# Optimization experiments

Measured on AMD Instinct MI355X. Metric: run time of the kernel, lower is better.

The kernel has to match this reference:

```python
import jax, jax.numpy as jnp
import numpy as np
import math

B, LQ, LK, D = 16, 2048, 2048, 64

def setup_inputs() -> dict:
    key = jax.random.key(0)
    kq, kk, kv, kn = jax.random.split(key, 4)
    q = jax.random.normal(kq, (B, LQ, D), dtype=jnp.float32)
    k = jax.random.normal(kk, (B, LK, D), dtype=jnp.float32)
    v = jax.random.normal(kv, (B, LK, D), dtype=jnp.float32)
    # valid lengths in [1, LK] so no row is fully masked
    valid_num = jax.random.randint(kn, (B,), 1, LK + 1, dtype=jnp.int32)
    return {"q": q, "k": k, "v": v, "valid_num": valid_num}

def reference(q, k, v, valid_num):
    d = q.shape[-1]
    # [B, LQ, LK] scores
    scores = jnp.einsum('bqd,bkd->bqk', q, k) / math.sqrt(d)
    # 1D valid_num -> same key mask for every query row (matches repeat_interleave)
    key_pos = jnp.arange(k.shape[1], dtype=valid_num.dtype)  # [LK]
    mask = key_pos[None, None, :] < valid_num[:, None, None]  # [B,1,LK] -> broadcast
    scores = jnp.where(mask, scores, -jnp.inf)
    attn = jax.nn.softmax(scores, axis=-1)
    # dropout p=0.0 -> identity (eval/deterministic reference)
    return jnp.einsum('bqk,bkd->bqd', attn, v)
```

## Files before the change

kernel.cpp:

```cpp
#include <hip/hip_runtime.h>


namespace {

constexpr int NB  = 16;
constexpr int SLQ = 2048;
constexpr int SLK = 2048;
constexpr int DH  = 64;
constexpr int KB  = 64;
constexpr int QB  = 64;

typedef _Float16 half8  __attribute__((ext_vector_type(8)));
typedef _Float16 half4  __attribute__((ext_vector_type(4)));
typedef _Float16 half2t __attribute__((ext_vector_type(2)));
typedef float    f32x4  __attribute__((ext_vector_type(4)));

__device__ inline half2t pkrtz(float a, float b) {
    return __builtin_bit_cast(half2t, __builtin_amdgcn_cvt_pkrtz(a, b));
}

__global__ __launch_bounds__(256)
void prepass(const float* __restrict__ kg, const float* __restrict__ vg,
             _Float16* __restrict__ k16, _Float16* __restrict__ v16t)
{
    __shared__ _Float16 VT[DH][72];
    const int t  = threadIdx.x;
    const int b  = blockIdx.x >> 5;
    const int kt = blockIdx.x & 31;

    {
        const size_t base = ((size_t)b * SLK + (size_t)kt * KB) * DH;
        const float* kp = kg + base + t * 16;
        f32x4 a0 = ((const f32x4*)kp)[0], a1 = ((const f32x4*)kp)[1];
        f32x4 a2 = ((const f32x4*)kp)[2], a3 = ((const f32x4*)kp)[3];
        union { half2t h2[8]; uint4 u[2]; } o;
        o.h2[0] = pkrtz(a0[0], a0[1]); o.h2[1] = pkrtz(a0[2], a0[3]);
        o.h2[2] = pkrtz(a1[0], a1[1]); o.h2[3] = pkrtz(a1[2], a1[3]);
        o.h2[4] = pkrtz(a2[0], a2[1]); o.h2[5] = pkrtz(a2[2], a2[3]);
        o.h2[6] = pkrtz(a3[0], a3[1]); o.h2[7] = pkrtz(a3[2], a3[3]);
        uint4* dst = (uint4*)(k16 + base + t * 16);
        dst[0] = o.u[0]; dst[1] = o.u[1];
    }
    {
        const int kr = t >> 2, d0 = (t & 3) * 16;
        const float* vp = vg + ((size_t)b * SLK + (size_t)kt * KB + kr) * DH + d0;
        f32x4 a0 = ((const f32x4*)vp)[0], a1 = ((const f32x4*)vp)[1];
        f32x4 a2 = ((const f32x4*)vp)[2], a3 = ((const f32x4*)vp)[3];
#pragma unroll
        for (int i = 0; i < 4; ++i) {
            VT[d0 + i][kr]      = (_Float16)a0[i];
            VT[d0 + 4 + i][kr]  = (_Float16)a1[i];
            VT[d0 + 8 + i][kr]  = (_Float16)a2[i];
            VT[d0 + 12 + i][kr] = (_Float16)a3[i];
        }
    }
    __syncthreads();
#pragma unroll
    for (int j = 0; j < 2; ++j) {
        const int chunk = t * 2 + j;
        const int d = chunk >> 3, c16 = chunk & 7;
        half8 hv = *(const half8*)&VT[d][c16 * 8];
        *(half8*)(v16t + ((size_t)b * DH + d) * SLK + (size_t)kt * KB + c16 * 8) = hv;
    }
}

__global__ __launch_bounds__(256)
void attn_fwd(const float* __restrict__ qg, const _Float16* __restrict__ k16,
              const _Float16* __restrict__ v16t, const int* __restrict__ vn,
              _Float16* __restrict__ ws_acc, float* __restrict__ ws_ml,
              int nsplit, int tps)
{
    __shared__ _Float16 Kl[KB * DH];
    __shared__ _Float16 Vt[DH * KB];

    const int t   = threadIdx.x;
    const int l   = t & 63;
    const int w   = t >> 6;
    const int q15 = l & 15;
    const int g   = l >> 4;
    const int swz = (q15 & 7) << 3;

    const int bid = blockIdx.x;
    int b, qt, s;
    if (nsplit == 8) {
        const int k4 = bid >> 8;
        s  = k4 & 7;
        b  = (((bid >> 4) & 15) + k4) & 15;
        qt = (bid & 15) | ((k4 >> 3) << 4);
    } else {
        b  = ((bid & 15) + 8 * (bid >> 8)) & 15;
        qt = (bid >> 4) & 31;
        s  = 0;
    }

    const int valid = vn[b];
    const int nkt   = (valid + KB - 1) / KB;
    const int kt0   = s * tps;
    if (kt0 >= nkt) return;
    const int kt1   = min(nkt, kt0 + tps);

    const int qrow = qt * QB + w * 16 + q15;

    const float QS = 0.18033688011112042f;

    half8 qf[2];
    {
        const float* qp = qg + ((size_t)b * SLQ + qrow) * DH;
#pragma unroll
        for (int ss = 0; ss < 2; ++ss) {
            const int d0 = 8 * g + 32 * ss;
            f32x4 x = *(const f32x4*)(qp + d0);
            f32x4 y = *(const f32x4*)(qp + d0 + 4);
            half8 h;
#pragma unroll
            for (int i = 0; i < 4; ++i) {
                h[i]     = (_Float16)(x[i] * QS);
                h[i + 4] = (_Float16)(y[i] * QS);
            }
            qf[ss] = h;
        }
    }

    f32x4 acc[4];
#pragma unroll
    for (int i = 0; i < 4; ++i) acc[i] = f32x4{0.f, 0.f, 0.f, 0.f};
    float m = -1e30f, lsum = 0.f;

    const _Float16* k16b = k16 + (size_t)b * SLK * DH;
    const _Float16* v16b = v16t + (size_t)b * DH * SLK;

    const int chunk = 2 * t;
    const int rr_   = chunk >> 3;
    const int cc_   = chunk & 7;
    const int scA   = (cc_ * 8) ^ ((rr_ & 7) << 3);
    const int scB   = scA ^ 8;
    const _Float16* ksrc = k16b + (size_t)chunk * 8;
    const _Float16* vsrc = v16b + (size_t)rr_ * SLK + cc_ * 8;

    uint4 ka, kb, va, vb;
#define PREFETCH(KT)                                                       \
    {                                                                      \
        const _Float16* kp = ksrc + (size_t)(KT) * (KB * DH);              \
        ka = ((const uint4*)kp)[0];                                        \
        kb = ((const uint4*)kp)[1];                                        \
        const _Float16* vp = vsrc + (size_t)(KT) * KB;                     \
        va = ((const uint4*)vp)[0];                                        \
        vb = ((const uint4*)vp)[1];                                        \
    }

    PREFETCH(kt0);

    for (int kt = kt0; kt < kt1; ++kt) {
        __syncthreads();

        *(uint4*)&Kl[rr_ * 64 + scA] = ka;
        *(uint4*)&Kl[rr_ * 64 + scB] = kb;
        *(uint4*)&Vt[rr_ * 64 + scA] = va;
        *(uint4*)&Vt[rr_ * 64 + scB] = vb;
        if (kt + 1 < kt1) PREFETCH(kt + 1);
        __syncthreads();

        f32x4 st[4];
        __builtin_amdgcn_s_setprio(1);
#pragma unroll
        for (int mt = 0; mt < 4; ++mt) {
            f32x4 c = f32x4{0.f, 0.f, 0.f, 0.f};
#pragma unroll
            for (int ss = 0; ss < 2; ++ss) {
                half8 a = *(const half8*)&Kl[(16 * mt + q15) * 64 + ((8 * g + 32 * ss) ^ swz)];
                c = __builtin_amdgcn_mfma_f32_16x16x32_f16(a, qf[ss], c, 0, 0, 0);
            }
            st[mt] = c;
        }
        __builtin_amdgcn_s_setprio(0);

        const int krem = valid - kt * KB;
        if (krem < KB) {
#pragma unroll
            for (int mt = 0; mt < 4; ++mt)
#pragma unroll
                for (int r = 0; r < 4; ++r)
                    if (16 * mt + 4 * g + r >= krem) st[mt][r] = -1e30f;
        }

        float x0 = fmaxf(fmaxf(st[0][0], st[0][1]), fmaxf(st[0][2], st[0][3]));
        float x1 = fmaxf(fmaxf(st[1][0], st[1][1]), fmaxf(st[1][2], st[1][3]));
        float x2 = fmaxf(fmaxf(st[2][0], st[2][1]), fmaxf(st[2][2], st[2][3]));
        float x3 = fmaxf(fmaxf(st[3][0], st[3][1]), fmaxf(st[3][2], st[3][3]));
        float tmax = fmaxf(fmaxf(x0, x1), fmaxf(x2, x3));
        tmax = fmaxf(tmax, __shfl_xor(tmax, 16));
        tmax = fmaxf(tmax, __shfl_xor(tmax, 32));

        if (!__all(tmax - m <= 12.0f)) {
            const float mn = fmaxf(m, tmax);
            const float sc = __builtin_amdgcn_exp2f(m - mn);
            lsum *= sc;
#pragma unroll
            for (int mt = 0; mt < 4; ++mt) acc[mt] *= sc;
            m = mn;
        }

        float p[4][4];
#pragma unroll
        for (int mt = 0; mt < 4; ++mt)
#pragma unroll
            for (int r = 0; r < 4; ++r)
                p[mt][r] = __builtin_amdgcn_exp2f(st[mt][r] - m);

        float s0 = (p[0][0] + p[0][1]) + (p[0][2] + p[0][3]);
        float s1 = (p[1][0] + p[1][1]) + (p[1][2] + p[1][3]);
        float s2 = (p[2][0] + p[2][1]) + (p[2][2] + p[2][3]);
        float s3 = (p[3][0] + p[3][1]) + (p[3][2] + p[3][3]);
        float ps = (s0 + s1) + (s2 + s3);
        ps += __shfl_xor(ps, 16);
        ps += __shfl_xor(ps, 32);
        lsum += ps;

        half2t pk[4][2];
#pragma unroll
        for (int mt = 0; mt < 4; ++mt)
#pragma unroll
            for (int rr = 0; rr < 2; ++rr)
                pk[mt][rr] = pkrtz(p[mt][2 * rr], p[mt][2 * rr + 1]);

        __builtin_amdgcn_s_setprio(1);
#pragma unroll
        for (int ss = 0; ss < 2; ++ss) {
            union { half2t h2[4]; half8 v; } bf;
            bf.h2[0] = pk[2 * ss][0];
            bf.h2[1] = pk[2 * ss][1];
            bf.h2[2] = pk[2 * ss + 1][0];
            bf.h2[3] = pk[2 * ss + 1][1];
#pragma unroll
            for (int mt = 0; mt < 4; ++mt) {
                union { half4 h4[2]; half8 v; } af;
                af.h4[0] = *(const half4*)&Vt[(16 * mt + q15) * 64 + ((32 * ss + 4 * g) ^ swz)];
                af.h4[1] = *(const half4*)&Vt[(16 * mt + q15) * 64 + ((32 * ss + 16 + 4 * g) ^ swz)];
                acc[mt] = __builtin_amdgcn_mfma_f32_16x16x32_f16(af.v, bf.v, acc[mt], 0, 0, 0);
            }
        }
        __builtin_amdgcn_s_setprio(0);
    }
#undef PREFETCH

    const float inv = 1.0f / lsum;
    const size_t row = (size_t)b * SLQ + qrow;
    _Float16* wp = ws_acc + ((size_t)s * NB * SLQ + row) * DH;
#pragma unroll
    for (int mt = 0; mt < 4; ++mt) {
        union { half2t h2[2]; uint2 u; } o;
        o.h2[0] = pkrtz(acc[mt][0] * inv, acc[mt][1] * inv);
        o.h2[1] = pkrtz(acc[mt][2] * inv, acc[mt][3] * inv);
        *(uint2*)(wp + 16 * mt + 4 * g) = o.u;
    }
    if (g == 0)
        *(float2*)(ws_ml + ((size_t)s * NB * SLQ + row) * 2) = make_float2(m, lsum);
}

__global__ __launch_bounds__(256)
void attn_combine(const _Float16* __restrict__ ws_acc, const float* __restrict__ ws_ml,
                  const int* __restrict__ vn, float* __restrict__ og,
                  int nsplit, int tps)
{
    const int tid = blockIdx.x * 256 + threadIdx.x;
    const int row = tid >> 2;
    const int dq  = (tid & 3) << 4;
    const int b   = row >> 11;

    const int valid = vn[b];
    const int nkt   = (valid + KB - 1) / KB;
    const int nact  = min(nsplit, (nkt + tps - 1) / tps);

    float M = -1e30f;
    for (int s = 0; s < nact; ++s)
        M = fmaxf(M, ws_ml[((size_t)s * NB * SLQ + row) * 2]);

    float L = 0.f;
    f32x4 o[4];
#pragma unroll
    for (int i = 0; i < 4; ++i) o[i] = f32x4{0.f, 0.f, 0.f, 0.f};

    for (int s = 0; s < nact; ++s) {
        const float2 ml = *(const float2*)(ws_ml + ((size_t)s * NB * SLQ + row) * 2);
        const float wl = __builtin_amdgcn_exp2f(ml.x - M) * ml.y;
        L += wl;
        const _Float16* ap = ws_acc + ((size_t)s * NB * SLQ + row) * DH + dq;
        half8 h0 = ((const half8*)ap)[0];
        half8 h1 = ((const half8*)ap)[1];
#pragma unroll
        for (int r = 0; r < 4; ++r) {
            o[0][r] += wl * (float)h0[r];
            o[1][r] += wl * (float)h0[4 + r];
            o[2][r] += wl * (float)h1[r];
            o[3][r] += wl * (float)h1[4 + r];
        }
    }

    const float inv = 1.0f / L;
    float* op = og + (size_t)row * DH + dq;
#pragma unroll
    for (int i = 0; i < 4; ++i) {
        f32x4 r = o[i] * inv;
        *(f32x4*)(op + 4 * i) = r;
    }
}

}

extern "C" void kernel_launch(void* const* d_in, const int* in_sizes, int n_in,
                              void* d_out, int out_size, void* d_ws, size_t ws_size,
                              hipStream_t stream)
{
    const float* q    = (const float*)d_in[0];
    const float* k    = (const float*)d_in[1];
    const float* v    = (const float*)d_in[2];
    const int*   vnum = (const int*)d_in[3];
    float* out = (float*)d_out;

    const size_t k16H  = (size_t)NB * SLK * DH;
    const size_t v16H  = k16H;
    const size_t rowsH = (size_t)NB * SLQ;

    int nsplit = 8;
    {
        const size_t need8 = (k16H + v16H + (size_t)8 * rowsH * DH) * 2
                           + (size_t)8 * rowsH * 2 * 4;
        if (ws_size < need8) nsplit = 1;
    }
    const int tps = (nsplit == 8) ? 4 : 32;

    _Float16* k16    = (_Float16*)d_ws;
    _Float16* v16t   = k16 + k16H;
    _Float16* ws_acc = v16t + v16H;
    float*    ws_ml  = (float*)(ws_acc + (size_t)nsplit * rowsH * DH);

    prepass<<<dim3(NB * (SLK / KB)), dim3(256), 0, stream>>>(k, v, k16, v16t);

    dim3 gfwd(nsplit == 8 ? 4096 : 512);
    attn_fwd<<<gfwd, dim3(256), 0, stream>>>(q, k16, v16t, vnum, ws_acc, ws_ml,
                                             nsplit, tps);

    attn_combine<<<dim3((NB * SLQ * 4) / 256), dim3(256), 0, stream>>>(
        ws_acc, ws_ml, vnum, out, nsplit, tps);
}
```

Before: 43.87 us.

## Pre-swizzle K/V tiles in prepass and double-buffer LDS to drop a barrier

The prepass now writes K and transposed V as contiguous 64x64 fp16 tiles with the LDS XOR swizzle already applied. The main kernel can then copy each tile linearly with coalesced uint4 loads and stores. LDS is double-buffered, so each iteration needs one __syncthreads instead of two. This removes per-tile address computation and a barrier, but doubles LDS use to 32 KB per block, which may reduce occupancy.

```diff
diff --git a/kernel.cpp b/kernel.cpp
--- a/kernel.cpp
+++ b/kernel.cpp
@@ -21,25 +21,30 @@
 
 __global__ __launch_bounds__(256)
 void prepass(const float* __restrict__ kg, const float* __restrict__ vg,
-             _Float16* __restrict__ k16, _Float16* __restrict__ v16t)
+             _Float16* __restrict__ kws, _Float16* __restrict__ vws)
 {
     __shared__ _Float16 VT[DH][72];
     const int t  = threadIdx.x;
     const int b  = blockIdx.x >> 5;
     const int kt = blockIdx.x & 31;
+    const size_t tileH = ((size_t)(b << 5) + kt) * 4096;
 
     {
-        const size_t base = ((size_t)b * SLK + (size_t)kt * KB) * DH;
-        const float* kp = kg + base + t * 16;
+        const float* kp = kg + ((size_t)b * SLK + (size_t)kt * KB) * DH + t * 16;
         f32x4 a0 = ((const f32x4*)kp)[0], a1 = ((const f32x4*)kp)[1];
         f32x4 a2 = ((const f32x4*)kp)[2], a3 = ((const f32x4*)kp)[3];
-        union { half2t h2[8]; uint4 u[2]; } o;
-        o.h2[0] = pkrtz(a0[0], a0[1]); o.h2[1] = pkrtz(a0[2], a0[3]);
-        o.h2[2] = pkrtz(a1[0], a1[1]); o.h2[3] = pkrtz(a1[2], a1[3]);
-        o.h2[4] = pkrtz(a2[0], a2[1]); o.h2[5] = pkrtz(a2[2], a2[3]);
-        o.h2[6] = pkrtz(a3[0], a3[1]); o.h2[7] = pkrtz(a3[2], a3[3]);
-        uint4* dst = (uint4*)(k16 + base + t * 16);
-        dst[0] = o.u[0]; dst[1] = o.u[1];
+        union { half2t h2[4]; uint4 u; } o0, o1;
+        o0.h2[0] = pkrtz(a0[0], a0[1]); o0.h2[1] = pkrtz(a0[2], a0[3]);
+        o0.h2[2] = pkrtz(a1[0], a1[1]); o0.h2[3] = pkrtz(a1[2], a1[3]);
+        o1.h2[0] = pkrtz(a2[0], a2[1]); o1.h2[1] = pkrtz(a2[2], a2[3]);
+        o1.h2[2] = pkrtz(a3[0], a3[1]); o1.h2[3] = pkrtz(a3[2], a3[3]);
+#pragma unroll
+        for (int j = 0; j < 2; ++j) {
+            const int n = 2 * t + j;
+            const int rr = n >> 3, c = n & 7;
+            const int dst = rr * 8 + (c ^ (rr & 7));
+            *(uint4*)(kws + tileH + (size_t)dst * 8) = j ? o1.u : o0.u;
+        }
     }
     {
         const int kr = t >> 2, d0 = (t & 3) * 16;
@@ -57,21 +62,21 @@
     __syncthreads();
 #pragma unroll
     for (int j = 0; j < 2; ++j) {
-        const int chunk = t * 2 + j;
-        const int d = chunk >> 3, c16 = chunk & 7;
-        half8 hv = *(const half8*)&VT[d][c16 * 8];
-        *(half8*)(v16t + ((size_t)b * DH + d) * SLK + (size_t)kt * KB + c16 * 8) = hv;
+        const int n = 2 * t + j;
+        const int d = n >> 3, c = n & 7;
+        const int dst = d * 8 + (c ^ (d & 7));
+        half8 hv = *(const half8*)&VT[d][c * 8];
+        *(half8*)(vws + tileH + (size_t)dst * 8) = hv;
     }
 }
 
 __global__ __launch_bounds__(256)
 void attn_fwd(const float* __restrict__ qg, const _Float16* __restrict__ k16,
-              const _Float16* __restrict__ v16t, const int* __restrict__ vn,
+              const _Float16* __restrict__ v16, const int* __restrict__ vn,
               _Float16* __restrict__ ws_acc, float* __restrict__ ws_ml,
               int nsplit, int tps)
 {
-    __shared__ _Float16 Kl[KB * DH];
-    __shared__ _Float16 Vt[DH * KB];
+    __shared__ __attribute__((aligned(16))) _Float16 KV[2][8192];
 
     const int t   = threadIdx.x;
     const int l   = t & 63;
@@ -126,39 +131,35 @@
     for (int i = 0; i < 4; ++i) acc[i] = f32x4{0.f, 0.f, 0.f, 0.f};
     float m = -1e30f, lsum = 0.f;
 
-    const _Float16* k16b = k16 + (size_t)b * SLK * DH;
-    const _Float16* v16b = v16t + (size_t)b * DH * SLK;
-
-    const int chunk = 2 * t;
-    const int rr_   = chunk >> 3;
-    const int cc_   = chunk & 7;
-    const int scA   = (cc_ * 8) ^ ((rr_ & 7) << 3);
-    const int scB   = scA ^ 8;
-    const _Float16* ksrc = k16b + (size_t)chunk * 8;
-    const _Float16* vsrc = v16b + (size_t)rr_ * SLK + cc_ * 8;
-
-    uint4 ka, kb, va, vb;
-#define PREFETCH(KT)                                                       \
-    {                                                                      \
-        const _Float16* kp = ksrc + (size_t)(KT) * (KB * DH);              \
-        ka = ((const uint4*)kp)[0];                                        \
-        kb = ((const uint4*)kp)[1];                                        \
-        const _Float16* vp = vsrc + (size_t)(KT) * KB;                     \
-        va = ((const uint4*)vp)[0];                                        \
-        vb = ((const uint4*)vp)[1];                                        \
-    }
-
-    PREFETCH(kt0);
+    const _Float16* kbase = k16 + (size_t)(b << 5) * 4096;
+    const _Float16* vbase = v16 + (size_t)(b << 5) * 4096;
+
+    uint4 rk0, rk1, rv0, rv1;
+#define LOADREGS(KT)                                                         \
+    {                                                                        \
+        const uint4* kp_ = (const uint4*)(kbase + (size_t)(KT) * 4096);      \
+        const uint4* vp_ = (const uint4*)(vbase + (size_t)(KT) * 4096);      \
+        rk0 = kp_[t]; rk1 = kp_[t + 256];                                    \
+        rv0 = vp_[t]; rv1 = vp_[t + 256];                                    \
+    }
+#define WRITEKV(CUR)                                                         \
+    {                                                                        \
+        uint4* kl_ = (uint4*)&KV[CUR][0];                                    \
+        uint4* vl_ = (uint4*)&KV[CUR][4096];                                 \
+        kl_[t] = rk0; kl_[t + 256] = rk1;                                    \
+        vl_[t] = rv0; vl_[t + 256] = rv1;                                    \
+    }
+
+    LOADREGS(kt0);
+    int cur = 0;
 
     for (int kt = kt0; kt < kt1; ++kt) {
+        WRITEKV(cur);
         __syncthreads();
-
-        *(uint4*)&Kl[rr_ * 64 + scA] = ka;
-        *(uint4*)&Kl[rr_ * 64 + scB] = kb;
-        *(uint4*)&Vt[rr_ * 64 + scA] = va;
-        *(uint4*)&Vt[rr_ * 64 + scB] = vb;
-        if (kt + 1 < kt1) PREFETCH(kt + 1);
-        __syncthreads();
+        if (kt + 1 < kt1) LOADREGS(kt + 1);
+
+        const _Float16* Kc = &KV[cur][0];
+        const _Float16* Vc = &KV[cur][4096];
 
         f32x4 st[4];
         __builtin_amdgcn_s_setprio(1);
@@ -167,7 +168,7 @@
             f32x4 c = f32x4{0.f, 0.f, 0.f, 0.f};
 #pragma unroll
             for (int ss = 0; ss < 2; ++ss) {
-                half8 a = *(const half8*)&Kl[(16 * mt + q15) * 64 + ((8 * g + 32 * ss) ^ swz)];
+                half8 a = *(const half8*)&Kc[(16 * mt + q15) * 64 + ((8 * g + 32 * ss) ^ swz)];
                 c = __builtin_amdgcn_mfma_f32_16x16x32_f16(a, qf[ss], c, 0, 0, 0);
             }
             st[mt] = c;
@@ -234,14 +235,16 @@
 #pragma unroll
             for (int mt = 0; mt < 4; ++mt) {
                 union { half4 h4[2]; half8 v; } af;
-                af.h4[0] = *(const half4*)&Vt[(16 * mt + q15) * 64 + ((32 * ss + 4 * g) ^ swz)];
-                af.h4[1] = *(const half4*)&Vt[(16 * mt + q15) * 64 + ((32 * ss + 16 + 4 * g) ^ swz)];
+                af.h4[0] = *(const half4*)&Vc[(16 * mt + q15) * 64 + ((32 * ss + 4 * g) ^ swz)];
+                af.h4[1] = *(const half4*)&Vc[(16 * mt + q15) * 64 + ((32 * ss + 16 + 4 * g) ^ swz)];
                 acc[mt] = __builtin_amdgcn_mfma_f32_16x16x32_f16(af.v, bf.v, acc[mt], 0, 0, 0);
             }
         }
         __builtin_amdgcn_s_setprio(0);
-    }
-#undef PREFETCH
+        cur ^= 1;
+    }
+#undef LOADREGS
+#undef WRITEKV
 
     const float inv = 1.0f / lsum;
     const size_t row = (size_t)b * SLQ + qrow;
```

Measured after the change: 43.62 us. About the same (-0.6%).
